# Optimization experiments

Measured on AMD Instinct MI355X. Metric: run time of the kernel, lower is better.

The kernel has to match this reference:

```python
import jax, jax.numpy as jnp
import numpy as np
from jax import lax

B, L, D_MODEL = 4, 512, 256
N_LAYERS = 6
EXPAND = 2
D_INNER = EXPAND * D_MODEL  # 512
D_STATE = 16
D_CONV = 4
DT_RANK = (D_MODEL + 15) // 16  # 16
EPS = 1e-5


def silu(x):
    return x * jax.nn.sigmoid(x)


def rmsnorm(x, w):
    var = jnp.mean(x * x, axis=-1, keepdims=True)
    return x * lax.rsqrt(var + EPS) * w


def setup_inputs() -> dict:
    key = jax.random.key(0)
    ks = jax.random.split(key, 12)
    s = lambda *sh: 0.02
    inp = {
        "x": jax.random.normal(ks[0], (B, L, D_MODEL), dtype=jnp.float32),
        "norm_w": jnp.ones((N_LAYERS, D_MODEL), jnp.float32),
        "W_in": jax.random.normal(ks[1], (N_LAYERS, 2 * D_INNER, D_MODEL), jnp.float32) * 0.02,
        "b_in": jnp.zeros((N_LAYERS, 2 * D_INNER), jnp.float32),
        "conv_w": jax.random.normal(ks[2], (N_LAYERS, D_INNER, D_CONV), jnp.float32) * 0.2,
        "W_x": jax.random.normal(ks[3], (N_LAYERS, DT_RANK + 2 * D_STATE, D_INNER), jnp.float32) * 0.02,
        "dt_w": jax.random.normal(ks[4], (N_LAYERS, D_INNER, DT_RANK), jnp.float32) * 0.1,
        "dt_b": jax.random.uniform(ks[5], (N_LAYERS, D_INNER), jnp.float32, -4.0, -2.0),
        "A_log": jnp.log(jnp.broadcast_to(jnp.arange(1, D_STATE + 1, dtype=jnp.float32), (N_LAYERS, D_INNER, D_STATE))),
        "D": jnp.ones((N_LAYERS, D_INNER), jnp.float32),
        "W_out": jax.random.normal(ks[6], (N_LAYERS, D_MODEL, D_INNER), jnp.float32) * 0.02,
        "b_out": jnp.zeros((N_LAYERS, D_MODEL), jnp.float32),
    }
    return inp


def mamba_block(x, W_in, b_in, conv_w, W_x, dt_w, dt_b, A_log, D, W_out, b_out):
    # input projection -> (B, L, 2*d_inner)
    xz = jnp.einsum("bld,ed->ble", x, W_in) + b_in
    xin, z = xz[..., :D_INNER], xz[..., D_INNER:]
    # depthwise causal conv over time (groups = d_inner, left pad d_conv-1)
    xc = lax.conv_general_dilated(
        xin.transpose(0, 2, 1),            # (B, C, L)
        conv_w[:, None, :],                # (C, 1, K)
        window_strides=(1,),
        padding=[(D_CONV - 1, 0)],
        feature_group_count=D_INNER,
        dimension_numbers=("NCH", "OIH", "NCH"),
    ).transpose(0, 2, 1)
    u = silu(xc)                           # (B, L, d_inner)
    # data-dependent dt, B, C
    xdbc = jnp.einsum("bld,rd->blr", u, W_x)
    dt = xdbc[..., :DT_RANK]
    Bm = xdbc[..., DT_RANK:DT_RANK + D_STATE]
    Cm = xdbc[..., DT_RANK + D_STATE:]
    delta = jax.nn.softplus(jnp.einsum("blr,dr->bld", dt, dt_w) + dt_b)
    A = -jnp.exp(A_log)                    # (d_inner, d_state)
    dA = jnp.exp(jnp.einsum("bld,dn->bldn", delta, A))
    dBu = jnp.einsum("bld,bln->bldn", delta * u, Bm)
    # selective scan over time
    def step(h, inp):
        dA_t, dBu_t, C_t = inp
        h = dA_t * h + dBu_t               # (B, d_inner, d_state)
        y_t = jnp.einsum("bdn,bn->bd", h, C_t)
        return h, y_t
    h0 = jnp.zeros((B, D_INNER, D_STATE), x.dtype)
    _, ys = lax.scan(step, h0, (dA.transpose(1, 0, 2, 3), dBu.transpose(1, 0, 2, 3), Cm.transpose(1, 0, 2)))
    y = ys.transpose(1, 0, 2) + u * D      # skip connection D*u
    y = y * silu(z)
    return jnp.einsum("bld,md->blm", y, W_out) + b_out


def reference(x, norm_w, W_in, b_in, conv_w, W_x, dt_w, dt_b, A_log, D, W_out, b_out):
    for i in range(N_LAYERS):
        x = x + mamba_block(rmsnorm(x, norm_w[i]), W_in[i], b_in[i], conv_w[i], W_x[i], dt_w[i], dt_b[i], A_log[i], D[i], W_out[i], b_out[i])
    return x
```

## Files before the change

kernel.cpp:

```cpp
#include <hip/hip_runtime.h>
#include <hip/hip_bf16.h>

#define B_SZ 4
#define L_SZ 512
#define D_MODEL 256
#define D_INNER 512
#define D_STATE 16
#define DT_RANK 16
#define N_LAYERS 6
#define BL (B_SZ * L_SZ)

typedef __bf16 bf16_t;
typedef __bf16 bf16x8 __attribute__((ext_vector_type(8)));
typedef __bf16 bf16x4 __attribute__((ext_vector_type(4)));
typedef float  f32x4  __attribute__((ext_vector_type(4)));

__device__ __forceinline__ float row_allreduce16(float x)
{
    int v;
    v = __builtin_amdgcn_mov_dpp(__float_as_int(x), 0x121, 0xf, 0xf, true);
    x += __int_as_float(v);
    v = __builtin_amdgcn_mov_dpp(__float_as_int(x), 0x122, 0xf, 0xf, true);
    x += __int_as_float(v);
    v = __builtin_amdgcn_mov_dpp(__float_as_int(x), 0x124, 0xf, 0xf, true);
    x += __int_as_float(v);
    v = __builtin_amdgcn_mov_dpp(__float_as_int(x), 0x128, 0xf, 0xf, true);
    x += __int_as_float(v);
    return x;
}

__global__ __launch_bounds__(256) void cast3_kernel(
    const float* __restrict__ s0, const float* __restrict__ s1,
    const float* __restrict__ s2, bf16_t* __restrict__ dst,
    int n0, int n1, int n2)
{
    int i = blockIdx.x * 256 + threadIdx.x;
    const float* s; int off;
    if (i < n0)            { s = s0; off = i; }
    else if (i < n0 + n1)  { s = s1; off = i - n0; }
    else if (i < n0+n1+n2) { s = s2; off = i - n0 - n1; }
    else return;
    const float4 v = *(const float4*)(s + (size_t)off * 4);
    bf16x4 o;
    o[0] = (bf16_t)v.x; o[1] = (bf16_t)v.y;
    o[2] = (bf16_t)v.z; o[3] = (bf16_t)v.w;
    *(bf16x4*)(dst + (size_t)i * 4) = o;
}

__global__ __launch_bounds__(256) void rmsnorm_kernel(
    const float* __restrict__ x, const float* __restrict__ w,
    bf16_t* __restrict__ o)
{
    int row  = blockIdx.x * 4 + (threadIdx.x >> 6);
    int lane = threadIdx.x & 63;
    const float4 v = *(const float4*)(x + (size_t)row * D_MODEL + lane * 4);
    float ss = v.x * v.x + v.y * v.y + v.z * v.z + v.w * v.w;
    #pragma unroll
    for (int off = 32; off; off >>= 1) ss += __shfl_xor(ss, off);
    float rs = rsqrtf(ss * (1.f / D_MODEL) + 1e-5f);
    const float4 wv = *(const float4*)(w + lane * 4);
    bf16x4 ov;
    ov[0] = (bf16_t)(v.x * rs * wv.x);
    ov[1] = (bf16_t)(v.y * rs * wv.y);
    ov[2] = (bf16_t)(v.z * rs * wv.z);
    ov[3] = (bf16_t)(v.w * rs * wv.w);
    *(bf16x4*)(o + (size_t)row * D_MODEL + lane * 4) = ov;
}

__global__ __launch_bounds__(256) void win_kernel(
    const bf16_t* __restrict__ A,
    const bf16_t* __restrict__ Bw,
    const float* __restrict__ bias,
    bf16_t* __restrict__ C,
    bf16_t* __restrict__ Z)
{
    constexpr int K = 256, BK = 64;
    __shared__ bf16_t As[64][K + 8];
    __shared__ bf16_t Bs[64][BK + 8];

    const int tid  = threadIdx.x;
    const int wave = tid >> 6, lane = tid & 63;
    const int wm = wave >> 1, wn = wave & 1;
    const int lm = lane & 15, quad = lane >> 4;
    const int m0 = blockIdx.y * 64, n0 = blockIdx.x * 64;

    #pragma unroll
    for (int i = tid; i < 64 * (K / 8); i += 256) {
        int r = i >> 5, c8 = i & 31;
        *(bf16x8*)&As[r][c8 * 8] =
            *(const bf16x8*)(A + (size_t)(m0 + r) * K + c8 * 8);
    }

    f32x4 acc[2][2] = {};
    for (int k0 = 0; k0 < K; k0 += BK) {
        #pragma unroll
        for (int i = tid; i < 64 * (BK / 8); i += 256) {
            int r = i >> 3, c8 = i & 7;
            *(bf16x8*)&Bs[r][c8 * 8] =
                *(const bf16x8*)(Bw + (size_t)(n0 + r) * K + k0 + c8 * 8);
        }
        __syncthreads();
        #pragma unroll
        for (int ks = 0; ks < 2; ++ks) {
            bf16x8 af[2], bfr[2];
            #pragma unroll
            for (int i = 0; i < 2; ++i)
                af[i] = *(const bf16x8*)&As[wm * 32 + i * 16 + lm][k0 + ks * 32 + quad * 8];
            #pragma unroll
            for (int j = 0; j < 2; ++j)
                bfr[j] = *(const bf16x8*)&Bs[wn * 32 + j * 16 + lm][ks * 32 + quad * 8];
            #pragma unroll
            for (int i = 0; i < 2; ++i)
                #pragma unroll
                for (int j = 0; j < 2; ++j)
                    acc[i][j] = __builtin_amdgcn_mfma_f32_16x16x32_bf16(
                        af[i], bfr[j], acc[i][j], 0, 0, 0);
        }
        __syncthreads();
    }

    if (n0 >= D_INNER) {
        #pragma unroll
        for (int i = 0; i < 2; ++i) {
            int rowbase = m0 + wm * 32 + i * 16 + quad * 4;
            #pragma unroll
            for (int j = 0; j < 2; ++j) {
                int col = n0 + wn * 32 + j * 16 + lm;
                bf16x4 o;
                #pragma unroll
                for (int r = 0; r < 4; ++r) {
                    float v = acc[i][j][r] + bias[col];
                    o[r] = (bf16_t)(v / (1.f + __expf(-v)));
                }
                *(bf16x4*)(Z + (size_t)(col - D_INNER) * BL + rowbase) = o;
            }
        }
        return;
    }

    #pragma unroll
    for (int i = 0; i < 2; ++i) {
        #pragma unroll
        for (int j = 0; j < 2; ++j) {
            int col = n0 + wn * 32 + j * 16 + lm;
            #pragma unroll
            for (int r = 0; r < 4; ++r) {
                int rowm = m0 + wm * 32 + i * 16 + quad * 4 + r;
                C[(size_t)rowm * D_INNER + col] = (bf16_t)(acc[i][j][r] + bias[col]);
            }
        }
    }
}

__global__ __launch_bounds__(256) void gemm_wout_norm(
    const bf16_t* __restrict__ A,
    const bf16_t* __restrict__ Bw,
    const float* __restrict__ bias,
    const float* __restrict__ R,
    const float* __restrict__ nw,
    float* __restrict__ C,
    bf16_t* __restrict__ Xn)
{
    constexpr int K = 512, BK = 64, BM = 16, BN = 256, LDK = BK + 8;
    __shared__ bf16_t As[BM][LDK];
    __shared__ bf16_t Bs[BN][LDK];
    __shared__ float rsum[BM][5];

    const int tid  = threadIdx.x;
    const int wave = tid >> 6, lane = tid & 63;
    const int lm = lane & 15, quad = lane >> 4;
    const int m0 = blockIdx.x * BM;

    f32x4 acc[4] = {};
    for (int k0 = 0; k0 < K; k0 += BK) {
        if (tid < BM * (BK / 8)) {
            int r = tid >> 3, c8 = tid & 7;
            *(bf16x8*)&As[r][c8 * 8] =
                *(const bf16x8*)(A + (size_t)(m0 + r) * K + k0 + c8 * 8);
        }
        #pragma unroll
        for (int i = tid; i < BN * (BK / 8); i += 256) {
            int r = i >> 3, c8 = i & 7;
            *(bf16x8*)&Bs[r][c8 * 8] =
                *(const bf16x8*)(Bw + (size_t)r * K + k0 + c8 * 8);
        }
        __syncthreads();
        #pragma unroll
        for (int ks = 0; ks < 2; ++ks) {
            bf16x8 af = *(const bf16x8*)&As[lm][ks * 32 + quad * 8];
            #pragma unroll
            for (int j = 0; j < 4; ++j) {
                bf16x8 bfr = *(const bf16x8*)&Bs[wave * 64 + j * 16 + lm][ks * 32 + quad * 8];
                acc[j] = __builtin_amdgcn_mfma_f32_16x16x32_bf16(af, bfr, acc[j], 0, 0, 0);
            }
        }
        __syncthreads();
    }

    float vv[4][4];
    #pragma unroll
    for (int j = 0; j < 4; ++j) {
        int col = wave * 64 + j * 16 + lm;
        float bj = bias[col];
        #pragma unroll
        for (int r = 0; r < 4; ++r) {
            int row = m0 + quad * 4 + r;
            vv[j][r] = acc[j][r] + bj + R[(size_t)row * D_MODEL + col];
        }
    }
    #pragma unroll
    for (int r = 0; r < 4; ++r) {
        float p = vv[0][r] * vv[0][r] + vv[1][r] * vv[1][r]
                + vv[2][r] * vv[2][r] + vv[3][r] * vv[3][r];
        p = row_allreduce16(p);
        if (lm == 0) rsum[quad * 4 + r][wave] = p;
    }
    __syncthreads();
    float rs[4];
    #pragma unroll
    for (int r = 0; r < 4; ++r) {
        int lr = quad * 4 + r;
        float tot = rsum[lr][0] + rsum[lr][1] + rsum[lr][2] + rsum[lr][3];
        rs[r] = rsqrtf(tot * (1.f / D_MODEL) + 1e-5f);
    }
    #pragma unroll
    for (int j = 0; j < 4; ++j) {
        int col = wave * 64 + j * 16 + lm;
        float wj = nw[col];
        #pragma unroll
        for (int r = 0; r < 4; ++r) {
            int row = m0 + quad * 4 + r;
            C[(size_t)row * D_MODEL + col] = vv[j][r];
            Xn[(size_t)row * D_MODEL + col] = (bf16_t)(vv[j][r] * rs[r] * wj);
        }
    }
}

__global__ __launch_bounds__(256) void wx_conv_kernel(
    const bf16_t* __restrict__ xzx,
    const float* __restrict__ cw,
    const bf16_t* __restrict__ Bw,
    const float* __restrict__ dt_w,
    const float* __restrict__ dt_b,
    bf16_t* __restrict__ uT,
    float* __restrict__ xdbcT,
    float* __restrict__ deltaT)
{
    constexpr int K = 512;
    __shared__ float  xs[19][516];
    __shared__ bf16_t us[16][520];
    __shared__ f32x4  part[4][3][64];
    __shared__ float  dtt[16][17];

    const int tid  = threadIdx.x;
    const int wave = tid >> 6, lane = tid & 63;
    const int lm = lane & 15, quad = lane >> 4;
    const int m0 = blockIdx.x * 16;

    for (int q = tid; q < 19 * 64; q += 256) {
        int rx = q >> 6, c8 = (q & 63) * 8;
        int mr = m0 - 3 + rx;
        if (mr >= 0) {
            bf16x8 v = *(const bf16x8*)(xzx + (size_t)mr * K + c8);
            #pragma unroll
            for (int e = 0; e < 8; ++e) xs[rx][c8 + e] = (float)v[e];
        } else {
            #pragma unroll
            for (int e = 0; e < 8; ++e) xs[rx][c8 + e] = 0.f;
        }
    }
    __syncthreads();

    #pragma unroll
    for (int it = 0; it < 8; ++it) {
        int item = tid + it * 256;
        int d = item >> 2, rg = item & 3;
        const float4 wv = *(const float4*)(cw + d * 4);
        bf16x4 ob;
        #pragma unroll
        for (int e = 0; e < 4; ++e) {
            int ro = rg * 4 + e;
            int t  = (m0 + ro) & (L_SZ - 1);
            float a = wv.w * xs[ro + 3][d];
            if (t >= 1) a += wv.z * xs[ro + 2][d];
            if (t >= 2) a += wv.y * xs[ro + 1][d];
            if (t >= 3) a += wv.x * xs[ro + 0][d];
            a = a / (1.f + __expf(-a));
            ob[e] = (bf16_t)a;
            us[ro][d] = (bf16_t)a;
        }
        *(bf16x4*)(uT + (size_t)d * BL + m0 + rg * 4) = ob;
    }
    __syncthreads();

    f32x4 acc[3] = {};
    const int kb = wave * 128 + quad * 8;
    #pragma unroll
    for (int ks = 0; ks < 4; ++ks) {
        int k0 = kb + ks * 32;
        bf16x8 af = *(const bf16x8*)&us[lm][k0];
        #pragma unroll
        for (int j = 0; j < 3; ++j) {
            bf16x8 bfr = *(const bf16x8*)(Bw + (size_t)(j * 16 + lm) * K + k0);
            acc[j] = __builtin_amdgcn_mfma_f32_16x16x32_bf16(af, bfr, acc[j], 0, 0, 0);
        }
    }
    #pragma unroll
    for (int j = 0; j < 3; ++j) part[wave][j][lane] = acc[j];
    __syncthreads();

    if (tid < 192) {
        int j = tid >> 6, l = tid & 63;
        f32x4 s = part[0][j][l];
        s += part[1][j][l];
        s += part[2][j][l];
        s += part[3][j][l];
        int col = j * 16 + (l & 15);
        float4 v = make_float4(s[0], s[1], s[2], s[3]);
        *(float4*)(xdbcT + (size_t)col * BL + m0 + (l >> 4) * 4) = v;
        if (j == 0) {
            #pragma unroll
            for (int e = 0; e < 4; ++e)
                dtt[(l >> 4) * 4 + e][l & 15] = s[e];
        }
    }
    __syncthreads();

    #pragma unroll
    for (int it = 0; it < 8; ++it) {
        int item = tid + it * 256;
        int d = item >> 2, tg = item & 3;
        const float4 w0 = *(const float4*)(dt_w + (size_t)d * 16 + 0);
        const float4 w1 = *(const float4*)(dt_w + (size_t)d * 16 + 4);
        const float4 w2 = *(const float4*)(dt_w + (size_t)d * 16 + 8);
        const float4 w3 = *(const float4*)(dt_w + (size_t)d * 16 + 12);
        const float bdt = dt_b[d];
        float4 o;
        #pragma unroll
        for (int e = 0; e < 4; ++e) {
            int t = tg * 4 + e;
            float a = bdt;
            a += dtt[t][0]  * w0.x + dtt[t][1]  * w0.y + dtt[t][2]  * w0.z + dtt[t][3]  * w0.w;
            a += dtt[t][4]  * w1.x + dtt[t][5]  * w1.y + dtt[t][6]  * w1.z + dtt[t][7]  * w1.w;
            a += dtt[t][8]  * w2.x + dtt[t][9]  * w2.y + dtt[t][10] * w2.z + dtt[t][11] * w2.w;
            a += dtt[t][12] * w3.x + dtt[t][13] * w3.y + dtt[t][14] * w3.z + dtt[t][15] * w3.w;
            ((float*)&o)[e] = (a > 20.f) ? a : __logf(1.f + __expf(a));
        }
        *(float4*)(deltaT + (size_t)d * BL + m0 + tg * 4) = o;
    }
}

__global__ __launch_bounds__(1024, 4) void scan_kernel(
    const float* __restrict__ xdbcT,
    const float* __restrict__ deltaT,
    const bf16_t* __restrict__ uT,
    const bf16_t* __restrict__ szT,
    const float* __restrict__ A_log,
    const float* __restrict__ Dv,
    bf16_t* __restrict__ y)
{
    constexpr int TC = 32;
    constexpr int NW = L_SZ / TC;

    int blk  = blockIdx.x;
    int b    = blk >> 7;
    int dg   = blk & 127;
    int wave = threadIdx.x >> 6;
    int lane = threadIdx.x & 63;
    int d    = dg * 4 + (lane >> 4);
    int n    = lane & 15;

    __shared__ float lds_Ap[NW][64];
    __shared__ float lds_he[NW][64];

    float Adn = -__expf(A_log[d * D_STATE + n]);
    int r0 = b * L_SZ + wave * TC;

    const float* Brow  = xdbcT  + (size_t)(DT_RANK + n) * BL;
    const float* Crow  = xdbcT  + (size_t)(DT_RANK + D_STATE + n) * BL;
    const float* drow  = deltaT + (size_t)d * BL;
    const bf16_t* urow = uT     + (size_t)d * BL;
    const bf16_t* zrow = szT    + (size_t)d * BL;

    {
        float h = 0.f, P = 1.f;
        #pragma unroll
        for (int j4 = 0; j4 < 8; ++j4) {
            int rb = r0 + j4 * 4;
            f32x4 dl = *(const f32x4*)(drow + rb);
            f32x4 Bv = *(const f32x4*)(Brow + rb);
            bf16x4 ub = *(const bf16x4*)(urow + rb);
            #pragma unroll
            for (int k = 0; k < 4; ++k) {
                float dA = __expf(dl[k] * Adn);
                h = dA * h + dl[k] * (float)ub[k] * Bv[k];
                P *= dA;
            }
        }
        lds_Ap[wave][lane] = P;
        lds_he[wave][lane] = h;
    }
    __syncthreads();

    float H = 0.f;
    for (int j = 0; j < wave; ++j)
        H = lds_Ap[j][lane] * H + lds_he[j][lane];

    float Dd = Dv[d];
    float h = H;
    #pragma unroll
    for (int g = 0; g < 2; ++g) {
        float py[16];
        #pragma unroll
        for (int j4 = 0; j4 < 4; ++j4) {
            int rb = r0 + g * 16 + j4 * 4;
            f32x4 dl = *(const f32x4*)(drow + rb);
            f32x4 Bv = *(const f32x4*)(Brow + rb);
            bf16x4 ub = *(const bf16x4*)(urow + rb);
            f32x4 Cc = *(const f32x4*)(Crow + rb);
            #pragma unroll
            for (int k = 0; k < 4; ++k) {
                float dA = __expf(dl[k] * Adn);
                h = dA * h + dl[k] * (float)ub[k] * Bv[k];
                py[j4 * 4 + k] = h * Cc[k];
            }
        }
        #pragma unroll
        for (int j = 0; j < 16; ++j)
            py[j] = row_allreduce16(py[j]);
        if (n == 0) {
            #pragma unroll
            for (int j4 = 0; j4 < 4; ++j4) {
                int rb = r0 + g * 16 + j4 * 4;
                bf16x4 ub = *(const bf16x4*)(urow + rb);
                bf16x4 zb = *(const bf16x4*)(zrow + rb);
                #pragma unroll
                for (int k = 0; k < 4; ++k) {
                    int row = rb + k;
                    y[(size_t)row * D_INNER + d] =
                        (bf16_t)((py[j4*4+k] + (float)ub[k] * Dd) * (float)zb[k]);
                }
            }
        }
    }
}

extern "C" void kernel_launch(void* const* d_in, const int* in_sizes, int n_in,
                              void* d_out, int out_size, void* d_ws, size_t ws_size,
                              hipStream_t stream)
{
    const float* x_in   = (const float*)d_in[0];
    const float* norm_w = (const float*)d_in[1];
    const float* W_in   = (const float*)d_in[2];
    const float* b_in   = (const float*)d_in[3];
    const float* conv_w = (const float*)d_in[4];
    const float* W_x    = (const float*)d_in[5];
    const float* dt_w   = (const float*)d_in[6];
    const float* dt_b   = (const float*)d_in[7];
    const float* A_log  = (const float*)d_in[8];
    const float* Dv     = (const float*)d_in[9];
    const float* W_out  = (const float*)d_in[10];
    const float* b_out  = (const float*)d_in[11];
    float* out = (float*)d_out;

    float* ws     = (float*)d_ws;
    float* xdbcT  = ws;
    float* deltaT = xdbcT + 48 * BL;
    bf16_t* bws   = (bf16_t*)(deltaT + D_INNER * BL);
    bf16_t* xz    = bws;
    bf16_t* uT    = xz    + BL * D_INNER;
    bf16_t* szT   = uT    + D_INNER * BL;
    bf16_t* xn_bf = szT   + D_INNER * BL;
    bf16_t* y_bf  = xn_bf + BL * D_MODEL;
    bf16_t* Wi_bf = y_bf  + BL * D_INNER;
    bf16_t* Wx_bf = Wi_bf + N_LAYERS * 2 * D_INNER * D_MODEL;
    bf16_t* Wo_bf = Wx_bf + N_LAYERS * 48 * D_INNER;

    {
        int n0 = N_LAYERS * 2 * D_INNER * D_MODEL / 4;
        int n1 = N_LAYERS * 48 * D_INNER / 4;
        int n2 = N_LAYERS * D_MODEL * D_INNER / 4;
        cast3_kernel<<<(n0 + n1 + n2 + 255) / 256, 256, 0, stream>>>(
            W_in, W_x, W_out, Wi_bf, n0, n1, n2);
    }

    rmsnorm_kernel<<<BL / 4, 256, 0, stream>>>(x_in, norm_w, xn_bf);

    for (int i = 0; i < N_LAYERS; ++i) {
        const float* xcur = (i == 0) ? x_in : out;

        win_kernel<<<dim3(1024 / 64, 2048 / 64), 256, 0, stream>>>(
            xn_bf, Wi_bf + (size_t)i * 2 * D_INNER * D_MODEL,
            b_in + i * 2 * D_INNER, xz, szT);

        wx_conv_kernel<<<BL / 16, 256, 0, stream>>>(
            xz, conv_w + i * D_INNER * 4,
            Wx_bf + (size_t)i * 48 * D_INNER,
            dt_w + (size_t)i * D_INNER * DT_RANK, dt_b + i * D_INNER,
            uT, xdbcT, deltaT);

        scan_kernel<<<512, 1024, 0, stream>>>(
            xdbcT, deltaT, uT, szT,
            A_log + (size_t)i * D_INNER * D_STATE, Dv + i * D_INNER, y_bf);

        const float* nw_next = norm_w + (size_t)((i + 1) % N_LAYERS) * D_MODEL;
        gemm_wout_norm<<<BL / 16, 256, 0, stream>>>(
            y_bf, Wo_bf + (size_t)i * D_MODEL * D_INNER,
            b_out + i * D_MODEL, xcur, nw_next, out, xn_bf);
    }
}
```

Baseline: 545.8 us.

## Fuse W_in projection GEMM into conv/W_x kernel, dropping xz round trip

Merges the input-projection GEMM into the conv + W_x + dt kernel. Each 16-row block recomputes the 3 preceding halo rows for the causal conv and keeps the xin half in shared memory, so the xz buffer no longer goes through global memory and one launch per layer disappears. In exchange, every block streams the full 1024x256 W_in matrix through shared memory in 16 chunks, about 128 blocks' worth of redundant weight traffic. It also does extra MFMA work for the halo rows and uses far fewer, thinner GEMM tiles than the old 64x64 tiling.

Result: slower. 666.3 us (+22.1%).

```diff
diff --git a/kernel.cpp b/kernel.cpp
--- a/kernel.cpp
+++ b/kernel.cpp
@@ -67,209 +67,86 @@
     *(bf16x4*)(o + (size_t)row * D_MODEL + lane * 4) = ov;
 }
 
-__global__ __launch_bounds__(256) void win_kernel(
+struct GemmSM { bf16_t As[19][264]; bf16_t Bs[64][264]; };
+struct PostSM { bf16_t us[16][520]; f32x4 part[4][3][64]; float dtt[16][17]; };
+union FusedSM { GemmSM g; PostSM p; };
+
+__global__ __launch_bounds__(256) void fused_win_conv(
     const bf16_t* __restrict__ A,
     const bf16_t* __restrict__ Bw,
     const float* __restrict__ bias,
-    bf16_t* __restrict__ C,
-    bf16_t* __restrict__ Z)
-{
-    constexpr int K = 256, BK = 64;
-    __shared__ bf16_t As[64][K + 8];
-    __shared__ bf16_t Bs[64][BK + 8];
-
-    const int tid  = threadIdx.x;
-    const int wave = tid >> 6, lane = tid & 63;
-    const int wm = wave >> 1, wn = wave & 1;
-    const int lm = lane & 15, quad = lane >> 4;
-    const int m0 = blockIdx.y * 64, n0 = blockIdx.x * 64;
-
-    #pragma unroll
-    for (int i = tid; i < 64 * (K / 8); i += 256) {
-        int r = i >> 5, c8 = i & 31;
-        *(bf16x8*)&As[r][c8 * 8] =
-            *(const bf16x8*)(A + (size_t)(m0 + r) * K + c8 * 8);
-    }
-
-    f32x4 acc[2][2] = {};
-    for (int k0 = 0; k0 < K; k0 += BK) {
-        #pragma unroll
-        for (int i = tid; i < 64 * (BK / 8); i += 256) {
-            int r = i >> 3, c8 = i & 7;
-            *(bf16x8*)&Bs[r][c8 * 8] =
-                *(const bf16x8*)(Bw + (size_t)(n0 + r) * K + k0 + c8 * 8);
-        }
-        __syncthreads();
-        #pragma unroll
-        for (int ks = 0; ks < 2; ++ks) {
-            bf16x8 af[2], bfr[2];
-            #pragma unroll
-            for (int i = 0; i < 2; ++i)
-                af[i] = *(const bf16x8*)&As[wm * 32 + i * 16 + lm][k0 + ks * 32 + quad * 8];
-            #pragma unroll
-            for (int j = 0; j < 2; ++j)
-                bfr[j] = *(const bf16x8*)&Bs[wn * 32 + j * 16 + lm][ks * 32 + quad * 8];
-            #pragma unroll
-            for (int i = 0; i < 2; ++i)
-                #pragma unroll
-                for (int j = 0; j < 2; ++j)
-                    acc[i][j] = __builtin_amdgcn_mfma_f32_16x16x32_bf16(
-                        af[i], bfr[j], acc[i][j], 0, 0, 0);
-        }
-        __syncthreads();
-    }
-
-    if (n0 >= D_INNER) {
-        #pragma unroll
-        for (int i = 0; i < 2; ++i) {
-            int rowbase = m0 + wm * 32 + i * 16 + quad * 4;
-            #pragma unroll
-            for (int j = 0; j < 2; ++j) {
-                int col = n0 + wn * 32 + j * 16 + lm;
-                bf16x4 o;
-                #pragma unroll
-                for (int r = 0; r < 4; ++r) {
-                    float v = acc[i][j][r] + bias[col];
-                    o[r] = (bf16_t)(v / (1.f + __expf(-v)));
-                }
-                *(bf16x4*)(Z + (size_t)(col - D_INNER) * BL + rowbase) = o;
-            }
-        }
-        return;
-    }
-
-    #pragma unroll
-    for (int i = 0; i < 2; ++i) {
-        #pragma unroll
-        for (int j = 0; j < 2; ++j) {
-            int col = n0 + wn * 32 + j * 16 + lm;
-            #pragma unroll
-            for (int r = 0; r < 4; ++r) {
-                int rowm = m0 + wm * 32 + i * 16 + quad * 4 + r;
-                C[(size_t)rowm * D_INNER + col] = (bf16_t)(acc[i][j][r] + bias[col]);
-            }
-        }
-    }
-}
-
-__global__ __launch_bounds__(256) void gemm_wout_norm(
-    const bf16_t* __restrict__ A,
-    const bf16_t* __restrict__ Bw,
-    const float* __restrict__ bias,
-    const float* __restrict__ R,
-    const float* __restrict__ nw,
-    float* __restrict__ C,
-    bf16_t* __restrict__ Xn)
-{
-    constexpr int K = 512, BK = 64, BM = 16, BN = 256, LDK = BK + 8;
-    __shared__ bf16_t As[BM][LDK];
-    __shared__ bf16_t Bs[BN][LDK];
-    __shared__ float rsum[BM][5];
-
-    const int tid  = threadIdx.x;
-    const int wave = tid >> 6, lane = tid & 63;
-    const int lm = lane & 15, quad = lane >> 4;
-    const int m0 = blockIdx.x * BM;
-
-    f32x4 acc[4] = {};
-    for (int k0 = 0; k0 < K; k0 += BK) {
-        if (tid < BM * (BK / 8)) {
-            int r = tid >> 3, c8 = tid & 7;
-            *(bf16x8*)&As[r][c8 * 8] =
-                *(const bf16x8*)(A + (size_t)(m0 + r) * K + k0 + c8 * 8);
-        }
-        #pragma unroll
-        for (int i = tid; i < BN * (BK / 8); i += 256) {
-            int r = i >> 3, c8 = i & 7;
-            *(bf16x8*)&Bs[r][c8 * 8] =
-                *(const bf16x8*)(Bw + (size_t)r * K + k0 + c8 * 8);
-        }
-        __syncthreads();
-        #pragma unroll
-        for (int ks = 0; ks < 2; ++ks) {
-            bf16x8 af = *(const bf16x8*)&As[lm][ks * 32 + quad * 8];
-            #pragma unroll
-            for (int j = 0; j < 4; ++j) {
-                bf16x8 bfr = *(const bf16x8*)&Bs[wave * 64 + j * 16 + lm][ks * 32 + quad * 8];
-                acc[j] = __builtin_amdgcn_mfma_f32_16x16x32_bf16(af, bfr, acc[j], 0, 0, 0);
-            }
-        }
-        __syncthreads();
-    }
-
-    float vv[4][4];
-    #pragma unroll
-    for (int j = 0; j < 4; ++j) {
-        int col = wave * 64 + j * 16 + lm;
-        float bj = bias[col];
-        #pragma unroll
-        for (int r = 0; r < 4; ++r) {
-            int row = m0 + quad * 4 + r;
-            vv[j][r] = acc[j][r] + bj + R[(size_t)row * D_MODEL + col];
-        }
-    }
-    #pragma unroll
-    for (int r = 0; r < 4; ++r) {
-        float p = vv[0][r] * vv[0][r] + vv[1][r] * vv[1][r]
-                + vv[2][r] * vv[2][r] + vv[3][r] * vv[3][r];
-        p = row_allreduce16(p);
-        if (lm == 0) rsum[quad * 4 + r][wave] = p;
-    }
-    __syncthreads();
-    float rs[4];
-    #pragma unroll
-    for (int r = 0; r < 4; ++r) {
-        int lr = quad * 4 + r;
-        float tot = rsum[lr][0] + rsum[lr][1] + rsum[lr][2] + rsum[lr][3];
-        rs[r] = rsqrtf(tot * (1.f / D_MODEL) + 1e-5f);
-    }
-    #pragma unroll
-    for (int j = 0; j < 4; ++j) {
-        int col = wave * 64 + j * 16 + lm;
-        float wj = nw[col];
-        #pragma unroll
-        for (int r = 0; r < 4; ++r) {
-            int row = m0 + quad * 4 + r;
-            C[(size_t)row * D_MODEL + col] = vv[j][r];
-            Xn[(size_t)row * D_MODEL + col] = (bf16_t)(vv[j][r] * rs[r] * wj);
-        }
-    }
-}
-
-__global__ __launch_bounds__(256) void wx_conv_kernel(
-    const bf16_t* __restrict__ xzx,
     const float* __restrict__ cw,
-    const bf16_t* __restrict__ Bw,
+    const bf16_t* __restrict__ Wx,
     const float* __restrict__ dt_w,
     const float* __restrict__ dt_b,
+    bf16_t* __restrict__ szT,
     bf16_t* __restrict__ uT,
     float* __restrict__ xdbcT,
     float* __restrict__ deltaT)
 {
-    constexpr int K = 512;
-    __shared__ float  xs[19][516];
-    __shared__ bf16_t us[16][520];
-    __shared__ f32x4  part[4][3][64];
-    __shared__ float  dtt[16][17];
+    constexpr int K = 256;
+    __shared__ float xs[19][516];
+    __shared__ FusedSM sm;
 
     const int tid  = threadIdx.x;
     const int wave = tid >> 6, lane = tid & 63;
     const int lm = lane & 15, quad = lane >> 4;
     const int m0 = blockIdx.x * 16;
 
-    for (int q = tid; q < 19 * 64; q += 256) {
-        int rx = q >> 6, c8 = (q & 63) * 8;
-        int mr = m0 - 3 + rx;
-        if (mr >= 0) {
-            bf16x8 v = *(const bf16x8*)(xzx + (size_t)mr * K + c8);
-            #pragma unroll
-            for (int e = 0; e < 8; ++e) xs[rx][c8 + e] = (float)v[e];
+    for (int i = tid; i < 19 * 32; i += 256) {
+        int r = i >> 5, c8 = i & 31;
+        int mr = m0 - 3 + r;
+        bf16x8 v;
+        #pragma unroll
+        for (int e = 0; e < 8; ++e) v[e] = (bf16_t)0.f;
+        if (mr >= 0) v = *(const bf16x8*)(A + (size_t)mr * K + c8 * 8);
+        *(bf16x8*)&sm.g.As[r][c8 * 8] = v;
+    }
+
+    for (int nc = 0; nc < 16; ++nc) {
+        #pragma unroll
+        for (int i = tid; i < 64 * 32; i += 256) {
+            int r = i >> 5, c8 = i & 31;
+            *(bf16x8*)&sm.g.Bs[r][c8 * 8] =
+                *(const bf16x8*)(Bw + (size_t)(nc * 64 + r) * K + c8 * 8);
+        }
+        __syncthreads();
+
+        const bool xhalf = (nc < 8);
+        f32x4 acc0 = {}, acc1 = {};
+        #pragma unroll
+        for (int ks = 0; ks < 8; ++ks) {
+            bf16x8 bfr = *(const bf16x8*)&sm.g.Bs[wave * 16 + lm][ks * 32 + quad * 8];
+            bf16x8 afm = *(const bf16x8*)&sm.g.As[3 + lm][ks * 32 + quad * 8];
+            acc0 = __builtin_amdgcn_mfma_f32_16x16x32_bf16(afm, bfr, acc0, 0, 0, 0);
+            if (xhalf) {
+                bf16x8 afh = *(const bf16x8*)&sm.g.As[lm][ks * 32 + quad * 8];
+                acc1 = __builtin_amdgcn_mfma_f32_16x16x32_bf16(afh, bfr, acc1, 0, 0, 0);
+            }
+        }
+
+        const int col = nc * 64 + wave * 16 + lm;
+        const float bj = bias[col];
+        if (xhalf) {
+            #pragma unroll
+            for (int r = 0; r < 4; ++r)
+                xs[3 + quad * 4 + r][col] = acc0[r] + bj;
+            if (quad == 0) {
+                #pragma unroll
+                for (int r = 0; r < 3; ++r)
+                    xs[r][col] = acc1[r] + bj;
+            }
         } else {
-            #pragma unroll
-            for (int e = 0; e < 8; ++e) xs[rx][c8 + e] = 0.f;
-        }
-    }
-    __syncthreads();
+            bf16x4 o;
+            #pragma unroll
+            for (int r = 0; r < 4; ++r) {
+                float v = acc0[r] + bj;
+                o[r] = (bf16_t)(v / (1.f + __expf(-v)));
+            }
+            *(bf16x4*)(szT + (size_t)(col - D_INNER) * BL + m0 + quad * 4) = o;
+        }
+        __syncthreads();
+    }
 
     #pragma unroll
     for (int it = 0; it < 8; ++it) {
@@ -287,41 +164,43 @@
             if (t >= 3) a += wv.x * xs[ro + 0][d];
             a = a / (1.f + __expf(-a));
             ob[e] = (bf16_t)a;
-            us[ro][d] = (bf16_t)a;
+            sm.p.us[ro][d] = (bf16_t)a;
         }
         *(bf16x4*)(uT + (size_t)d * BL + m0 + rg * 4) = ob;
     }
     __syncthreads();
 
-    f32x4 acc[3] = {};
-    const int kb = wave * 128 + quad * 8;
-    #pragma unroll
-    for (int ks = 0; ks < 4; ++ks) {
-        int k0 = kb + ks * 32;
-        bf16x8 af = *(const bf16x8*)&us[lm][k0];
-        #pragma unroll
-        for (int j = 0; j < 3; ++j) {
-            bf16x8 bfr = *(const bf16x8*)(Bw + (size_t)(j * 16 + lm) * K + k0);
-            acc[j] = __builtin_amdgcn_mfma_f32_16x16x32_bf16(af, bfr, acc[j], 0, 0, 0);
-        }
-    }
-    #pragma unroll
-    for (int j = 0; j < 3; ++j) part[wave][j][lane] = acc[j];
+    {
+        f32x4 acc[3] = {};
+        const int kb = wave * 128 + quad * 8;
+        #pragma unroll
+        for (int ks = 0; ks < 4; ++ks) {
+            int k0 = kb + ks * 32;
+            bf16x8 af = *(const bf16x8*)&sm.p.us[lm][k0];
+            #pragma unroll
+            for (int j = 0; j < 3; ++j) {
+                bf16x8 bfr = *(const bf16x8*)(Wx + (size_t)(j * 16 + lm) * D_INNER + k0);
+                acc[j] = __builtin_amdgcn_mfma_f32_16x16x32_bf16(af, bfr, acc[j], 0, 0, 0);
+            }
+        }
+        #pragma unroll
+        for (int j = 0; j < 3; ++j) sm.p.part[wave][j][lane] = acc[j];
+    }
     __syncthreads();
 
     if (tid < 192) {
         int j = tid >> 6, l = tid & 63;
-        f32x4 s = part[0][j][l];
-        s += part[1][j][l];
-        s += part[2][j][l];
-        s += part[3][j][l];
+        f32x4 s = sm.p.part[0][j][l];
+        s += sm.p.part[1][j][l];
+        s += sm.p.part[2][j][l];
+        s += sm.p.part[3][j][l];
         int col = j * 16 + (l & 15);
         float4 v = make_float4(s[0], s[1], s[2], s[3]);
         *(float4*)(xdbcT + (size_t)col * BL + m0 + (l >> 4) * 4) = v;
         if (j == 0) {
             #pragma unroll
             for (int e = 0; e < 4; ++e)
-                dtt[(l >> 4) * 4 + e][l & 15] = s[e];
+                sm.p.dtt[(l >> 4) * 4 + e][l & 15] = s[e];
         }
     }
     __syncthreads();
@@ -340,13 +219,101 @@
         for (int e = 0; e < 4; ++e) {
             int t = tg * 4 + e;
             float a = bdt;
-            a += dtt[t][0]  * w0.x + dtt[t][1]  * w0.y + dtt[t][2]  * w0.z + dtt[t][3]  * w0.w;
-            a += dtt[t][4]  * w1.x + dtt[t][5]  * w1.y + dtt[t][6]  * w1.z + dtt[t][7]  * w1.w;
-            a += dtt[t][8]  * w2.x + dtt[t][9]  * w2.y + dtt[t][10] * w2.z + dtt[t][11] * w2.w;
-            a += dtt[t][12] * w3.x + dtt[t][13] * w3.y + dtt[t][14] * w3.z + dtt[t][15] * w3.w;
+            a += sm.p.dtt[t][0]  * w0.x + sm.p.dtt[t][1]  * w0.y
+               + sm.p.dtt[t][2]  * w0.z + sm.p.dtt[t][3]  * w0.w;
+            a += sm.p.dtt[t][4]  * w1.x + sm.p.dtt[t][5]  * w1.y
+               + sm.p.dtt[t][6]  * w1.z + sm.p.dtt[t][7]  * w1.w;
+            a += sm.p.dtt[t][8]  * w2.x + sm.p.dtt[t][9]  * w2.y
+               + sm.p.dtt[t][10] * w2.z + sm.p.dtt[t][11] * w2.w;
+            a += sm.p.dtt[t][12] * w3.x + sm.p.dtt[t][13] * w3.y
+               + sm.p.dtt[t][14] * w3.z + sm.p.dtt[t][15] * w3.w;
             ((float*)&o)[e] = (a > 20.f) ? a : __logf(1.f + __expf(a));
         }
         *(float4*)(deltaT + (size_t)d * BL + m0 + tg * 4) = o;
+    }
+}
+
+__global__ __launch_bounds__(256) void gemm_wout_norm(
+    const bf16_t* __restrict__ A,
+    const bf16_t* __restrict__ Bw,
+    const float* __restrict__ bias,
+    const float* __restrict__ R,
+    const float* __restrict__ nw,
+    float* __restrict__ C,
+    bf16_t* __restrict__ Xn)
+{
+    constexpr int K = 512, BK = 64, BM = 16, BN = 256, LDK = BK + 8;
+    __shared__ bf16_t As[BM][LDK];
+    __shared__ bf16_t Bs[BN][LDK];
+    __shared__ float rsum[BM][5];
+
+    const int tid  = threadIdx.x;
+    const int wave = tid >> 6, lane = tid & 63;
+    const int lm = lane & 15, quad = lane >> 4;
+    const int m0 = blockIdx.x * BM;
+
+    f32x4 acc[4] = {};
+    for (int k0 = 0; k0 < K; k0 += BK) {
+        if (tid < BM * (BK / 8)) {
+            int r = tid >> 3, c8 = tid & 7;
+            *(bf16x8*)&As[r][c8 * 8] =
+                *(const bf16x8*)(A + (size_t)(m0 + r) * K + k0 + c8 * 8);
+        }
+        #pragma unroll
+        for (int i = tid; i < BN * (BK / 8); i += 256) {
+            int r = i >> 3, c8 = i & 7;
+            *(bf16x8*)&Bs[r][c8 * 8] =
+                *(const bf16x8*)(Bw + (size_t)r * K + k0 + c8 * 8);
+        }
+        __syncthreads();
+        #pragma unroll
+        for (int ks = 0; ks < 2; ++ks) {
+            bf16x8 af = *(const bf16x8*)&As[lm][ks * 32 + quad * 8];
+            #pragma unroll
+            for (int j = 0; j < 4; ++j) {
+                bf16x8 bfr = *(const bf16x8*)&Bs[wave * 64 + j * 16 + lm][ks * 32 + quad * 8];
+                acc[j] = __builtin_amdgcn_mfma_f32_16x16x32_bf16(af, bfr, acc[j], 0, 0, 0);
+            }
+        }
+        __syncthreads();
+    }
+
+    float vv[4][4];
+    #pragma unroll
+    for (int j = 0; j < 4; ++j) {
+        int col = wave * 64 + j * 16 + lm;
+        float bj = bias[col];
+        #pragma unroll
+        for (int r = 0; r < 4; ++r) {
+            int row = m0 + quad * 4 + r;
+            vv[j][r] = acc[j][r] + bj + R[(size_t)row * D_MODEL + col];
+        }
+    }
+    #pragma unroll
+    for (int r = 0; r < 4; ++r) {
+        float p = vv[0][r] * vv[0][r] + vv[1][r] * vv[1][r]
+                + vv[2][r] * vv[2][r] + vv[3][r] * vv[3][r];
+        p = row_allreduce16(p);
+        if (lm == 0) rsum[quad * 4 + r][wave] = p;
+    }
+    __syncthreads();
+    float rs[4];
+    #pragma unroll
+    for (int r = 0; r < 4; ++r) {
+        int lr = quad * 4 + r;
+        float tot = rsum[lr][0] + rsum[lr][1] + rsum[lr][2] + rsum[lr][3];
+        rs[r] = rsqrtf(tot * (1.f / D_MODEL) + 1e-5f);
+    }
+    #pragma unroll
+    for (int j = 0; j < 4; ++j) {
+        int col = wave * 64 + j * 16 + lm;
+        float wj = nw[col];
+        #pragma unroll
+        for (int r = 0; r < 4; ++r) {
+            int row = m0 + quad * 4 + r;
+            C[(size_t)row * D_MODEL + col] = vv[j][r];
+            Xn[(size_t)row * D_MODEL + col] = (bf16_t)(vv[j][r] * rs[r] * wj);
+        }
     }
 }
 
@@ -467,8 +434,7 @@
     float* xdbcT  = ws;
     float* deltaT = xdbcT + 48 * BL;
     bf16_t* bws   = (bf16_t*)(deltaT + D_INNER * BL);
-    bf16_t* xz    = bws;
-    bf16_t* uT    = xz    + BL * D_INNER;
+    bf16_t* uT    = bws;
     bf16_t* szT   = uT    + D_INNER * BL;
     bf16_t* xn_bf = szT   + D_INNER * BL;
     bf16_t* y_bf  = xn_bf + BL * D_MODEL;
@@ -489,15 +455,13 @@
     for (int i = 0; i < N_LAYERS; ++i) {
         const float* xcur = (i == 0) ? x_in : out;
 
-        win_kernel<<<dim3(1024 / 64, 2048 / 64), 256, 0, stream>>>(
+        fused_win_conv<<<BL / 16, 256, 0, stream>>>(
             xn_bf, Wi_bf + (size_t)i * 2 * D_INNER * D_MODEL,
-            b_in + i * 2 * D_INNER, xz, szT);
-
-        wx_conv_kernel<<<BL / 16, 256, 0, stream>>>(
-            xz, conv_w + i * D_INNER * 4,
+            b_in + i * 2 * D_INNER,
+            conv_w + i * D_INNER * 4,
             Wx_bf + (size_t)i * 48 * D_INNER,
             dt_w + (size_t)i * D_INNER * DT_RANK, dt_b + i * D_INNER,
-            uT, xdbcT, deltaT);
+            szT, uT, xdbcT, deltaT);
 
         scan_kernel<<<512, 1024, 0, stream>>>(
             xdbcT, deltaT, uT, szT,
```
